# Optimization experiments

Measured on AMD Instinct MI355X. Metric: run time of the kernel, lower is better.

The kernel has to match this reference:

```python
import jax, jax.numpy as jnp
import numpy as np

HIDDEN = 1024


def setup_inputs() -> dict:
    key = jax.random.key(0)
    ks = jax.random.split(key, 9)
    B, S, Kq, H = 16, 4096, 64, HIDDEN
    scale = 1.0 / np.sqrt(H)
    return {
        "queries": jax.random.normal(ks[0], (B, Kq, H), jnp.float32),
        "keys": jax.random.normal(ks[1], (B, S, H), jnp.float32),
        "values": jax.random.normal(ks[2], (B, S, H), jnp.float32),
        "Wq": jax.random.normal(ks[3], (H, H), jnp.float32) * scale,
        "bq": jax.random.normal(ks[4], (H,), jnp.float32) * 0.02,
        "Wk": jax.random.normal(ks[5], (H, H), jnp.float32) * scale,
        "bk": jax.random.normal(ks[6], (H,), jnp.float32) * 0.02,
        "Wv": jax.random.normal(ks[7], (H, H), jnp.float32) * scale,
        "bv": jax.random.normal(ks[8], (H,), jnp.float32) * 0.02,
    }


def reference(queries, keys, values, Wq, bq, Wk, bk, Wv, bv):
    H = Wq.shape[0]
    scaling = jax.lax.rsqrt(jnp.asarray(H, queries.dtype))
    # torch Linear: x @ W^T + b
    q = queries @ Wq.T + bq            # (B, Kq, H)
    k = keys @ Wk.T + bk               # (B, S, H)
    v = values @ Wv.T + bv             # (B, S, H)
    # scores: k @ q^T -> (B, S, Kq), softmax over seq_len axis (dim=1)
    scores = jnp.einsum('bsh,bqh->bsq', k, q) * scaling
    attention_weights = jax.nn.softmax(scores, axis=1)
    # context: attn^T @ v -> (B, Kq, H)
    context = jnp.einsum('bsq,bsh->bqh', attention_weights, v)
    return context, attention_weights
```

## Files before the change

kernel.cpp:

```cpp
#include <hip/hip_runtime.h>
#include <hip/hip_bf16.h>

#define H 1024
#define SEQ 4096
#define BQ 64
#define NB 16

typedef float f32x4 __attribute__((ext_vector_type(4)));
typedef __bf16 bf16x8 __attribute__((ext_vector_type(8)));

__device__ __forceinline__ void split_bf16(const float* x, bf16x8& hi, bf16x8& lo)
{
    #pragma unroll
    for (int i = 0; i < 8; ++i) {
        float v = x[i];
        __bf16 h = (__bf16)v;
        hi[i] = h;
        lo[i] = (__bf16)(v - (float)h);
    }
}

__device__ __forceinline__ void gload_lds16(const float* g, void* lds)
{
    __builtin_amdgcn_global_load_lds(
        (const __attribute__((address_space(1))) void*)g,
        (__attribute__((address_space(3))) void*)lds, 16, 0, 0);
}

template<int MODE>
__global__ __launch_bounds__(512)
void gemm_bt_512(const float* __restrict__ A, const float* __restrict__ Bm,
                 const float* __restrict__ bias, float* __restrict__ C,
                 __bf16* __restrict__ Nhi, __bf16* __restrict__ Nlo, float scale)
{
    const int m0 = blockIdx.x * 64;
    const int n0 = blockIdx.y * 64;
    const int t   = threadIdx.x;
    const int w   = t >> 6;
    const int wm  = w & 3;
    const int kh  = w >> 2;
    const int l   = t & 63;
    const int row = l & 15;
    const int kg  = l >> 4;

    const float* ap = A + (size_t)(m0 + wm * 16 + row) * H + kh * 512 + kg * 8;
    const float* bp = Bm + (size_t)(n0 + row) * H + kh * 512 + kg * 8;

    f32x4 acc[4] = {};
    for (int k0 = 0; k0 < 512; k0 += 32) {
        float a8[8];
        *reinterpret_cast<float4*>(&a8[0]) = *reinterpret_cast<const float4*>(ap + k0);
        *reinterpret_cast<float4*>(&a8[4]) = *reinterpret_cast<const float4*>(ap + k0 + 4);
        bf16x8 ahi, alo;
        split_bf16(a8, ahi, alo);
        #pragma unroll
        for (int j = 0; j < 4; ++j) {
            float b8[8];
            const float* bjp = bp + (size_t)j * 16 * H + k0;
            *reinterpret_cast<float4*>(&b8[0]) = *reinterpret_cast<const float4*>(bjp);
            *reinterpret_cast<float4*>(&b8[4]) = *reinterpret_cast<const float4*>(bjp + 4);
            bf16x8 bhi, blo;
            split_bf16(b8, bhi, blo);
            acc[j] = __builtin_amdgcn_mfma_f32_16x16x32_bf16(ahi, bhi, acc[j], 0, 0, 0);
            acc[j] = __builtin_amdgcn_mfma_f32_16x16x32_bf16(ahi, blo, acc[j], 0, 0, 0);
            acc[j] = __builtin_amdgcn_mfma_f32_16x16x32_bf16(alo, bhi, acc[j], 0, 0, 0);
        }
    }

    __shared__ f32x4 red[4][4][64];
    if (kh == 1) {
        #pragma unroll
        for (int j = 0; j < 4; ++j) red[wm][j][l] = acc[j];
    }
    __syncthreads();
    if (kh == 0) {
        #pragma unroll
        for (int j = 0; j < 4; ++j) {
            f32x4 s = acc[j] + red[wm][j][l];
            int n = n0 + j * 16 + row;
            if (MODE == 0) {
                float bb = bias ? bias[n] : 0.f;
                #pragma unroll
                for (int r = 0; r < 4; ++r) {
                    int m = m0 + wm * 16 + kg * 4 + r;
                    C[(size_t)m * H + n] = s[r] * scale + bb;
                }
            } else {
                #pragma unroll
                for (int r = 0; r < 4; ++r) {
                    int m = m0 + wm * 16 + kg * 4 + r;
                    float v = s[r] * scale;
                    __bf16 hi = (__bf16)v;
                    Nhi[(size_t)m * H + n] = hi;
                    Nlo[(size_t)m * H + n] = (__bf16)(v - (float)hi);
                }
            }
        }
    }
}

__global__ __launch_bounds__(256)
void transpose_k(const float* __restrict__ Wk, float* __restrict__ WkT)
{
    __shared__ float tile[64][65];
    const int k0 = blockIdx.x * 64;
    const int n0 = blockIdx.y * 64;
    const int t  = threadIdx.x;
    const int c4 = (t & 15) * 4;
    const int r  = t >> 4;
    #pragma unroll
    for (int p = 0; p < 4; ++p) {
        float4 v = *reinterpret_cast<const float4*>(&Wk[(size_t)(k0 + r + 16 * p) * H + n0 + c4]);
        tile[r + 16 * p][c4 + 0] = v.x;
        tile[r + 16 * p][c4 + 1] = v.y;
        tile[r + 16 * p][c4 + 2] = v.z;
        tile[r + 16 * p][c4 + 3] = v.w;
    }
    __syncthreads();
    #pragma unroll
    for (int p = 0; p < 4; ++p) {
        int rr = r + 16 * p;
        float4 o;
        o.x = tile[c4 + 0][rr];
        o.y = tile[c4 + 1][rr];
        o.z = tile[c4 + 2][rr];
        o.w = tile[c4 + 3][rr];
        *reinterpret_cast<float4*>(&WkT[(size_t)(n0 + rr) * H + k0 + c4]) = o;
    }
}

__global__ __launch_bounds__(256)
void cvec_kernel(const float* __restrict__ q, const float* __restrict__ bk,
                 float* __restrict__ cvec, float scale)
{
    int r = blockIdx.x * 4 + (threadIdx.x >> 6);
    int l = threadIdx.x & 63;
    float s = 0.f;
    #pragma unroll
    for (int i = 0; i < 16; ++i)
        s += q[(size_t)r * H + l + 64 * i] * bk[l + 64 * i];
    #pragma unroll
    for (int off = 32; off; off >>= 1)
        s += __shfl_down(s, off);
    if (l == 0) cvec[r] = s * scale;
}

__global__ __launch_bounds__(512)
void scores_mfma(const float* __restrict__ keys,
                 const __bf16* __restrict__ Nhi, const __bf16* __restrict__ Nlo,
                 const float* __restrict__ cvec, float* __restrict__ scores,
                 float* __restrict__ pmax, float* __restrict__ psum)
{
    const int id = blockIdx.x;
    const int x  = id & 7;
    const int m  = id >> 3;
    const int b  = 2 * x + (m >> 5);
    const int ch = m & 31;
    const int s0 = ch * 128;

    const int t   = threadIdx.x;
    const int w   = t >> 6;
    const int l   = t & 63;
    const int row = l & 15;
    const int kg  = l >> 4;

    __shared__ __bf16 nshH[64][16][8];
    __shared__ __bf16 nshL[64][16][8];
    __shared__ float redm[8][64];

    const float* ka = keys + ((size_t)b * SEQ + s0 + w * 16 + row) * H + kg * 8;
    const __bf16* nhb = Nhi + (size_t)b * BQ * H;
    const __bf16* nlb = Nlo + (size_t)b * BQ * H;

    const int sqi = (t >> 4) & 31;
    const int skb = t & 15;
    const int ssl = skb ^ (sqi & 7);

    f32x4 acc[4] = {};
    for (int c = 0; c < 8; ++c) {
        const int kc = c * 128;
        float4 kr[8];
        #pragma unroll
        for (int ii = 0; ii < 4; ++ii) {
            kr[2 * ii + 0] = *reinterpret_cast<const float4*>(ka + kc + ii * 32);
            kr[2 * ii + 1] = *reinterpret_cast<const float4*>(ka + kc + ii * 32 + 4);
        }
        bf16x8 nh[2], nl[2];
        #pragma unroll
        for (int rep = 0; rep < 2; ++rep) {
            size_t go = (size_t)(rep * 32 + sqi) * H + kc + skb * 8;
            nh[rep] = *reinterpret_cast<const bf16x8*>(nhb + go);
            nl[rep] = *reinterpret_cast<const bf16x8*>(nlb + go);
        }
        __syncthreads();
        #pragma unroll
        for (int rep = 0; rep < 2; ++rep) {
            *reinterpret_cast<bf16x8*>(&nshH[rep * 32 + sqi][ssl][0]) = nh[rep];
            *reinterpret_cast<bf16x8*>(&nshL[rep * 32 + sqi][ssl][0]) = nl[rep];
        }
        __syncthreads();
        #pragma unroll
        for (int ii = 0; ii < 4; ++ii) {
            float a8[8];
            *reinterpret_cast<float4*>(&a8[0]) = kr[2 * ii + 0];
            *reinterpret_cast<float4*>(&a8[4]) = kr[2 * ii + 1];
            bf16x8 ahi, alo;
            split_bf16(a8, ahi, alo);
            const int kb = ii * 4 + kg;
            const int slot = kb ^ (row & 7);
            #pragma unroll
            for (int j = 0; j < 4; ++j) {
                const int qi = j * 16 + row;
                bf16x8 bhi = *reinterpret_cast<const bf16x8*>(&nshH[qi][slot][0]);
                bf16x8 blo = *reinterpret_cast<const bf16x8*>(&nshL[qi][slot][0]);
                acc[j] = __builtin_amdgcn_mfma_f32_16x16x32_bf16(ahi, bhi, acc[j], 0, 0, 0);
                acc[j] = __builtin_amdgcn_mfma_f32_16x16x32_bf16(ahi, blo, acc[j], 0, 0, 0);
                acc[j] = __builtin_amdgcn_mfma_f32_16x16x32_bf16(alo, bhi, acc[j], 0, 0, 0);
            }
        }
    }

    #pragma unroll
    for (int j = 0; j < 4; ++j) {
        int qi = j * 16 + row;
        float cv = cvec[b * BQ + qi];
        #pragma unroll
        for (int r = 0; r < 4; ++r) {
            acc[j][r] += cv;
            int s = s0 + w * 16 + kg * 4 + r;
            scores[((size_t)b * SEQ + s) * BQ + qi] = acc[j][r];
        }
    }
    float mj[4];
    #pragma unroll
    for (int j = 0; j < 4; ++j) {
        float mm = fmaxf(fmaxf(acc[j][0], acc[j][1]), fmaxf(acc[j][2], acc[j][3]));
        mm = fmaxf(mm, __shfl_xor(mm, 16));
        mm = fmaxf(mm, __shfl_xor(mm, 32));
        mj[j] = mm;
    }
    __syncthreads();
    if (kg == 0) {
        #pragma unroll
        for (int j = 0; j < 4; ++j) redm[w][j * 16 + row] = mj[j];
    }
    __syncthreads();
    float Mj[4];
    #pragma unroll
    for (int j = 0; j < 4; ++j) {
        const int qi = j * 16 + row;
        float M = redm[0][qi];
        #pragma unroll
        for (int ww = 1; ww < 8; ++ww) M = fmaxf(M, redm[ww][qi]);
        Mj[j] = M;
    }
    float sj[4];
    #pragma unroll
    for (int j = 0; j < 4; ++j) {
        float s = 0.f;
        #pragma unroll
        for (int r = 0; r < 4; ++r) s += __expf(acc[j][r] - Mj[j]);
        s += __shfl_xor(s, 16);
        s += __shfl_xor(s, 32);
        sj[j] = s;
    }
    __syncthreads();
    if (kg == 0) {
        #pragma unroll
        for (int j = 0; j < 4; ++j) redm[w][j * 16 + row] = sj[j];
    }
    __syncthreads();
    if (w == 0 && kg == 0) {
        #pragma unroll
        for (int j = 0; j < 4; ++j) {
            const int qi = j * 16 + row;
            float ss = 0.f;
            #pragma unroll
            for (int ww = 0; ww < 8; ++ww) ss += redm[ww][qi];
            pmax[((size_t)b * 32 + ch) * 64 + qi] = Mj[j];
            psum[((size_t)b * 32 + ch) * 64 + qi] = ss;
        }
    }
}

__global__ void sm_combine(const float* __restrict__ pmax,
                           const float* __restrict__ psum,
                           float* __restrict__ gstat)
{
    int b  = blockIdx.x;
    int qi = threadIdx.x;
    float m = -1e30f;
    for (int c = 0; c < 32; ++c)
        m = fmaxf(m, pmax[((size_t)b * 32 + c) * 64 + qi]);
    float s = 0.f;
    for (int c = 0; c < 32; ++c)
        s += psum[((size_t)b * 32 + c) * 64 + qi] *
             __expf(pmax[((size_t)b * 32 + c) * 64 + qi] - m);
    gstat[(size_t)b * 64 + qi] = m;
    gstat[(size_t)(NB + b) * 64 + qi] = 1.f / s;
}

__global__ __launch_bounds__(256)
void sm_norm(float* __restrict__ attn, const float* __restrict__ gstat,
             __hip_bfloat16* __restrict__ abfT)
{
    __shared__ float tile[64][133];
    const int b  = blockIdx.y;
    const int ch = blockIdx.x;
    const int t  = threadIdx.x;
    const int qi = t & 63;
    const int g  = t >> 6;
    const float M   = gstat[(size_t)b * 64 + qi];
    const float inv = gstat[(size_t)(NB + b) * 64 + qi];
    float* sb = attn + ((size_t)b * SEQ + ch * 128) * BQ;
    #pragma unroll 8
    for (int i = 0; i < 32; ++i) {
        int sl = g + i * 4;
        size_t idx = (size_t)sl * BQ + qi;
        float w = __expf(sb[idx] - M) * inv;
        sb[idx] = w;
        tile[qi][sl] = w;
    }
    __syncthreads();
    const int qo = t >> 2;
    const int c  = (t & 3) * 32;
    __hip_bfloat16* dst = abfT + ((size_t)(b * BQ + qo)) * SEQ + ch * 128 + c;
    #pragma unroll
    for (int v = 0; v < 4; ++v) {
        bf16x8 w8;
        #pragma unroll
        for (int e = 0; e < 8; ++e)
            w8[e] = (__bf16)tile[qo][c + v * 8 + e];
        *reinterpret_cast<bf16x8*>(dst + v * 8) = w8;
    }
}

template<int SC>
__global__ __launch_bounds__(256)
void tmat_mfma(const __hip_bfloat16* __restrict__ abfT,
               const float* __restrict__ values,
               float* __restrict__ Tpart)
{
    const int i  = blockIdx.x;
    const int h0 = ((i >> 3) & 7) * 128;
    const int g  = (i & 7) + 8 * (i >> 6);
    const int b  = g / SC;
    const int sc = g % SC;
    const int schunk = SEQ / SC;

    const int w   = threadIdx.x >> 6;
    const int l   = threadIdx.x & 63;
    const int row = l & 15;
    const int kg  = l >> 4;
    const int sbase = sc * schunk;

    __shared__ float vlds[2][32][128];

    const __hip_bfloat16* ap = abfT + ((size_t)b * BQ + row) * SEQ + sbase + kg * 8;
    const float* vb = values + ((size_t)b * SEQ + sbase) * H + h0;

    const int nk = schunk / 32;

    #define STAGE(buf, k0)                                                     \
        {                                                                      \
            _Pragma("unroll")                                                  \
            for (int ii = 0; ii < 4; ++ii) {                                   \
                int elem = w * 1024 + ii * 256 + l * 4;                        \
                int k    = elem >> 7;                                          \
                int cc   = elem & 127;                                         \
                int csw  = cc ^ ((k >> 3) << 4);                               \
                const float* src = vb + (size_t)((k0) + k) * H + csw;          \
                gload_lds16(src, (void*)(&vlds[buf][0][0] + w * 1024 + ii * 256)); \
            }                                                                  \
        }

    f32x4 acc[4][2] = {};
    STAGE(0, 0);
    __syncthreads();

    for (int ks = 0; ks < nk; ++ks) {
        const int buf = ks & 1;
        if (ks + 1 < nk) STAGE(buf ^ 1, (ks + 1) * 32);
        const int k0 = ks * 32;
        bf16x8 a[4];
        #pragma unroll
        for (int q = 0; q < 4; ++q)
            a[q] = *reinterpret_cast<const bf16x8*>(ap + (size_t)q * 16 * SEQ + k0);
        #pragma unroll
        for (int j = 0; j < 2; ++j) {
            const int col = (w * 32 + j * 16 + row) ^ (kg << 4);
            float b8[8];
            #pragma unroll
            for (int e = 0; e < 8; ++e)
                b8[e] = vlds[buf][kg * 8 + e][col];
            bf16x8 bhi, blo;
            split_bf16(b8, bhi, blo);
            #pragma unroll
            for (int q = 0; q < 4; ++q) {
                acc[q][j] = __builtin_amdgcn_mfma_f32_16x16x32_bf16(a[q], bhi, acc[q][j], 0, 0, 0);
                acc[q][j] = __builtin_amdgcn_mfma_f32_16x16x32_bf16(a[q], blo, acc[q][j], 0, 0, 0);
            }
        }
        __syncthreads();
    }
    #undef STAGE

    float* tp = Tpart + ((size_t)sc * NB + b) * BQ * H;
    #pragma unroll
    for (int q = 0; q < 4; ++q) {
        #pragma unroll
        for (int j = 0; j < 2; ++j) {
            int h = h0 + w * 32 + j * 16 + row;
            #pragma unroll
            for (int r = 0; r < 4; ++r) {
                int qi = q * 16 + kg * 4 + r;
                tp[(size_t)qi * H + h] = acc[q][j][r];
            }
        }
    }
}

template<int SC>
__global__ __launch_bounds__(256)
void tsum_kernel(float* __restrict__ Tpart)
{
    const size_t stride = (size_t)NB * BQ * H;
    size_t i = ((size_t)blockIdx.x * 256 + threadIdx.x) * 4;
    f32x4 s = *reinterpret_cast<const f32x4*>(Tpart + i);
    #pragma unroll
    for (int p = 1; p < SC; ++p)
        s += *reinterpret_cast<const f32x4*>(Tpart + p * stride + i);
    *reinterpret_cast<f32x4*>(Tpart + i) = s;
}

extern "C" void kernel_launch(void* const* d_in, const int* in_sizes, int n_in,
                              void* d_out, int out_size, void* d_ws, size_t ws_size,
                              hipStream_t stream)
{
    const float* queries = (const float*)d_in[0];
    const float* keys    = (const float*)d_in[1];
    const float* values  = (const float*)d_in[2];
    const float* Wq = (const float*)d_in[3];
    const float* bq = (const float*)d_in[4];
    const float* Wk = (const float*)d_in[5];
    const float* bk = (const float*)d_in[6];
    const float* Wv = (const float*)d_in[7];
    const float* bv = (const float*)d_in[8];

    float* out     = (float*)d_out;
    float* context = out;
    float* attn    = out + (size_t)NB * BQ * H;

    const int SC = (ws_size >= (41ull << 20)) ? 8 : 2;

    char* ws = (char*)d_ws;
    float* q     = (float*)ws;
    float* WkT   = (float*)(ws + (4ull << 20));
    __bf16* Nhi  = (__bf16*)(ws + (8ull << 20));
    __bf16* Nlo  = (__bf16*)(ws + (10ull << 20));
    float* Tpart = (float*)ws;
    __hip_bfloat16* abfT = (__hip_bfloat16*)(ws + (size_t)SC * (4ull << 20));
    char* smalls = ws + (size_t)SC * (4ull << 20) + (8ull << 20);
    float* cvec  = (float*)smalls;
    float* gstat = (float*)(smalls + (64u << 10));
    float* pmax  = (float*)(smalls + (128u << 10));
    float* psum  = (float*)(smalls + (512u << 10));

    const float scale = 0.03125f;

    transpose_k<<<dim3(16, 16), 256, 0, stream>>>(Wk, WkT);
    gemm_bt_512<0><<<dim3(16, 16), 512, 0, stream>>>(
        queries, Wq, bq, q, nullptr, nullptr, 1.0f);
    gemm_bt_512<1><<<dim3(16, 16), 512, 0, stream>>>(
        q, WkT, nullptr, nullptr, Nhi, Nlo, scale);
    cvec_kernel<<<256, 256, 0, stream>>>(q, bk, cvec, scale);
    scores_mfma<<<512, 512, 0, stream>>>(keys, Nhi, Nlo, cvec, attn, pmax, psum);
    sm_combine<<<NB, 64, 0, stream>>>(pmax, psum, gstat);
    sm_norm<<<dim3(32, NB), 256, 0, stream>>>(attn, gstat, abfT);
    if (SC == 8) tmat_mfma<8><<<8 * NB * 8, 256, 0, stream>>>(abfT, values, Tpart);
    else         tmat_mfma<2><<<8 * NB * 2, 256, 0, stream>>>(abfT, values, Tpart);
    if (SC == 8) tsum_kernel<8><<<1024, 256, 0, stream>>>(Tpart);
    else         tsum_kernel<2><<<1024, 256, 0, stream>>>(Tpart);
    gemm_bt_512<0><<<dim3(16, 16), 512, 0, stream>>>(
        Tpart, Wv, bv, context, nullptr, nullptr, 1.0f);
}
```

Baseline: 284.8 us.

## Fuse small kernels, drop Wk transpose, double-buffer scores k-loop

```diff
diff --git a/kernel.cpp b/kernel.cpp
--- a/kernel.cpp
+++ b/kernel.cpp
@@ -27,11 +27,12 @@
         (__attribute__((address_space(3))) void*)lds, 16, 0, 0);
 }
 
-template<int MODE>
+template<bool CVEC>
 __global__ __launch_bounds__(512)
 void gemm_bt_512(const float* __restrict__ A, const float* __restrict__ Bm,
                  const float* __restrict__ bias, float* __restrict__ C,
-                 __bf16* __restrict__ Nhi, __bf16* __restrict__ Nlo, float scale)
+                 float scale, const float* __restrict__ bk,
+                 float* __restrict__ cvec, float cscale)
 {
     const int m0 = blockIdx.x * 64;
     const int n0 = blockIdx.y * 64;
@@ -74,78 +75,99 @@
     }
     __syncthreads();
     if (kh == 0) {
+        float p[4] = {0.f, 0.f, 0.f, 0.f};
         #pragma unroll
         for (int j = 0; j < 4; ++j) {
             f32x4 s = acc[j] + red[wm][j][l];
             int n = n0 + j * 16 + row;
-            if (MODE == 0) {
-                float bb = bias ? bias[n] : 0.f;
+            float bb = bias ? bias[n] : 0.f;
+            float bkv = CVEC ? bk[n] : 0.f;
+            #pragma unroll
+            for (int r = 0; r < 4; ++r) {
+                int m = m0 + wm * 16 + kg * 4 + r;
+                float o = s[r] * scale + bb;
+                C[(size_t)m * H + n] = o;
+                if (CVEC) p[r] += o * bkv;
+            }
+        }
+        if (CVEC) {
+            #pragma unroll
+            for (int r = 0; r < 4; ++r) {
                 #pragma unroll
-                for (int r = 0; r < 4; ++r) {
-                    int m = m0 + wm * 16 + kg * 4 + r;
-                    C[(size_t)m * H + n] = s[r] * scale + bb;
-                }
-            } else {
+                for (int off = 1; off < 16; off <<= 1)
+                    p[r] += __shfl_xor(p[r], off);
+            }
+            if (row == 0) {
                 #pragma unroll
-                for (int r = 0; r < 4; ++r) {
-                    int m = m0 + wm * 16 + kg * 4 + r;
-                    float v = s[r] * scale;
-                    __bf16 hi = (__bf16)v;
-                    Nhi[(size_t)m * H + n] = hi;
-                    Nlo[(size_t)m * H + n] = (__bf16)(v - (float)hi);
-                }
-            }
-        }
-    }
-}
-
-__global__ __launch_bounds__(256)
-void transpose_k(const float* __restrict__ Wk, float* __restrict__ WkT)
-{
-    __shared__ float tile[64][65];
-    const int k0 = blockIdx.x * 64;
+                for (int r = 0; r < 4; ++r)
+                    atomicAdd(&cvec[m0 + wm * 16 + kg * 4 + r], p[r] * cscale);
+            }
+        }
+    }
+}
+
+__global__ __launch_bounds__(512)
+void ngemm_direct(const float* __restrict__ A, const float* __restrict__ Wk,
+                  __bf16* __restrict__ Nhi, __bf16* __restrict__ Nlo, float scale)
+{
+    const int m0 = blockIdx.x * 64;
     const int n0 = blockIdx.y * 64;
-    const int t  = threadIdx.x;
-    const int c4 = (t & 15) * 4;
-    const int r  = t >> 4;
-    #pragma unroll
-    for (int p = 0; p < 4; ++p) {
-        float4 v = *reinterpret_cast<const float4*>(&Wk[(size_t)(k0 + r + 16 * p) * H + n0 + c4]);
-        tile[r + 16 * p][c4 + 0] = v.x;
-        tile[r + 16 * p][c4 + 1] = v.y;
-        tile[r + 16 * p][c4 + 2] = v.z;
-        tile[r + 16 * p][c4 + 3] = v.w;
-    }
-    __syncthreads();
-    #pragma unroll
-    for (int p = 0; p < 4; ++p) {
-        int rr = r + 16 * p;
-        float4 o;
-        o.x = tile[c4 + 0][rr];
-        o.y = tile[c4 + 1][rr];
-        o.z = tile[c4 + 2][rr];
-        o.w = tile[c4 + 3][rr];
-        *reinterpret_cast<float4*>(&WkT[(size_t)(n0 + rr) * H + k0 + c4]) = o;
-    }
-}
-
-__global__ __launch_bounds__(256)
-void cvec_kernel(const float* __restrict__ q, const float* __restrict__ bk,
-                 float* __restrict__ cvec, float scale)
-{
-    int r = blockIdx.x * 4 + (threadIdx.x >> 6);
-    int l = threadIdx.x & 63;
-    float s = 0.f;
-    #pragma unroll
-    for (int i = 0; i < 16; ++i)
-        s += q[(size_t)r * H + l + 64 * i] * bk[l + 64 * i];
-    #pragma unroll
-    for (int off = 32; off; off >>= 1)
-        s += __shfl_down(s, off);
-    if (l == 0) cvec[r] = s * scale;
-}
-
-__global__ __launch_bounds__(512)
+    const int t   = threadIdx.x;
+    const int w   = t >> 6;
+    const int wm  = w & 3;
+    const int kh  = w >> 2;
+    const int l   = t & 63;
+    const int row = l & 15;
+    const int kg  = l >> 4;
+
+    const float* ap = A + (size_t)(m0 + wm * 16 + row) * H + kh * 512 + kg * 8;
+    const float* bp = Wk + (size_t)(kh * 512 + kg * 8) * H + n0 + row;
+
+    f32x4 acc[4] = {};
+    for (int k0 = 0; k0 < 512; k0 += 32) {
+        float a8[8];
+        *reinterpret_cast<float4*>(&a8[0]) = *reinterpret_cast<const float4*>(ap + k0);
+        *reinterpret_cast<float4*>(&a8[4]) = *reinterpret_cast<const float4*>(ap + k0 + 4);
+        bf16x8 ahi, alo;
+        split_bf16(a8, ahi, alo);
+        #pragma unroll
+        for (int j = 0; j < 4; ++j) {
+            float b8[8];
+            #pragma unroll
+            for (int e = 0; e < 8; ++e)
+                b8[e] = bp[(size_t)(k0 + e) * H + j * 16];
+            bf16x8 bhi, blo;
+            split_bf16(b8, bhi, blo);
+            acc[j] = __builtin_amdgcn_mfma_f32_16x16x32_bf16(ahi, bhi, acc[j], 0, 0, 0);
+            acc[j] = __builtin_amdgcn_mfma_f32_16x16x32_bf16(ahi, blo, acc[j], 0, 0, 0);
+            acc[j] = __builtin_amdgcn_mfma_f32_16x16x32_bf16(alo, bhi, acc[j], 0, 0, 0);
+        }
+    }
+
+    __shared__ f32x4 red[4][4][64];
+    if (kh == 1) {
+        #pragma unroll
+        for (int j = 0; j < 4; ++j) red[wm][j][l] = acc[j];
+    }
+    __syncthreads();
+    if (kh == 0) {
+        #pragma unroll
+        for (int j = 0; j < 4; ++j) {
+            f32x4 s = acc[j] + red[wm][j][l];
+            int n = n0 + j * 16 + row;
+            #pragma unroll
+            for (int r = 0; r < 4; ++r) {
+                int m = m0 + wm * 16 + kg * 4 + r;
+                float v = s[r] * scale;
+                __bf16 hi = (__bf16)v;
+                Nhi[(size_t)m * H + n] = hi;
+                Nlo[(size_t)m * H + n] = (__bf16)(v - (float)hi);
+            }
+        }
+    }
+}
+
+__global__ __launch_bounds__(512, 4)
 void scores_mfma(const float* __restrict__ keys,
                  const __bf16* __restrict__ Nhi, const __bf16* __restrict__ Nlo,
                  const float* __restrict__ cvec, float* __restrict__ scores,
@@ -164,46 +186,54 @@
     const int row = l & 15;
     const int kg  = l >> 4;
 
-    __shared__ __bf16 nshH[64][16][8];
-    __shared__ __bf16 nshL[64][16][8];
+    __shared__ __bf16 nshH[2][64][8][8];
+    __shared__ __bf16 nshL[2][64][8][8];
     __shared__ float redm[8][64];
 
     const float* ka = keys + ((size_t)b * SEQ + s0 + w * 16 + row) * H + kg * 8;
     const __bf16* nhb = Nhi + (size_t)b * BQ * H;
     const __bf16* nlb = Nlo + (size_t)b * BQ * H;
 
-    const int sqi = (t >> 4) & 31;
-    const int skb = t & 15;
+    const int sqi = t >> 3;
+    const int skb = t & 7;
     const int ssl = skb ^ (sqi & 7);
 
+    float4 kr[2][4];
+    bf16x8 nh[2], nl[2];
+    #pragma unroll
+    for (int ii = 0; ii < 2; ++ii) {
+        kr[0][2 * ii + 0] = *reinterpret_cast<const float4*>(ka + ii * 32);
+        kr[0][2 * ii + 1] = *reinterpret_cast<const float4*>(ka + ii * 32 + 4);
+    }
+    {
+        size_t go = (size_t)sqi * H + skb * 8;
+        nh[0] = *reinterpret_cast<const bf16x8*>(nhb + go);
+        nl[0] = *reinterpret_cast<const bf16x8*>(nlb + go);
+    }
+
     f32x4 acc[4] = {};
-    for (int c = 0; c < 8; ++c) {
-        const int kc = c * 128;
-        float4 kr[8];
-        #pragma unroll
-        for (int ii = 0; ii < 4; ++ii) {
-            kr[2 * ii + 0] = *reinterpret_cast<const float4*>(ka + kc + ii * 32);
-            kr[2 * ii + 1] = *reinterpret_cast<const float4*>(ka + kc + ii * 32 + 4);
-        }
-        bf16x8 nh[2], nl[2];
-        #pragma unroll
-        for (int rep = 0; rep < 2; ++rep) {
-            size_t go = (size_t)(rep * 32 + sqi) * H + kc + skb * 8;
-            nh[rep] = *reinterpret_cast<const bf16x8*>(nhb + go);
-            nl[rep] = *reinterpret_cast<const bf16x8*>(nlb + go);
-        }
+    #pragma unroll
+    for (int c = 0; c < 16; ++c) {
+        const int buf = c & 1;
+        *reinterpret_cast<bf16x8*>(&nshH[buf][sqi][ssl][0]) = nh[buf];
+        *reinterpret_cast<bf16x8*>(&nshL[buf][sqi][ssl][0]) = nl[buf];
         __syncthreads();
-        #pragma unroll
-        for (int rep = 0; rep < 2; ++rep) {
-            *reinterpret_cast<bf16x8*>(&nshH[rep * 32 + sqi][ssl][0]) = nh[rep];
-            *reinterpret_cast<bf16x8*>(&nshL[rep * 32 + sqi][ssl][0]) = nl[rep];
-        }
-        __syncthreads();
-        #pragma unroll
-        for (int ii = 0; ii < 4; ++ii) {
+        if (c < 15) {
+            const int kc = (c + 1) * 64;
+            #pragma unroll
+            for (int ii = 0; ii < 2; ++ii) {
+                kr[buf ^ 1][2 * ii + 0] = *reinterpret_cast<const float4*>(ka + kc + ii * 32);
+                kr[buf ^ 1][2 * ii + 1] = *reinterpret_cast<const float4*>(ka + kc + ii * 32 + 4);
+            }
+            size_t go = (size_t)sqi * H + kc + skb * 8;
+            nh[buf ^ 1] = *reinterpret_cast<const bf16x8*>(nhb + go);
+            nl[buf ^ 1] = *reinterpret_cast<const bf16x8*>(nlb + go);
+        }
+        #pragma unroll
+        for (int ii = 0; ii < 2; ++ii) {
             float a8[8];
-            *reinterpret_cast<float4*>(&a8[0]) = kr[2 * ii + 0];
-            *reinterpret_cast<float4*>(&a8[4]) = kr[2 * ii + 1];
+            *reinterpret_cast<float4*>(&a8[0]) = kr[buf][2 * ii + 0];
+            *reinterpret_cast<float4*>(&a8[4]) = kr[buf][2 * ii + 1];
             bf16x8 ahi, alo;
             split_bf16(a8, ahi, alo);
             const int kb = ii * 4 + kg;
@@ -211,8 +241,8 @@
             #pragma unroll
             for (int j = 0; j < 4; ++j) {
                 const int qi = j * 16 + row;
-                bf16x8 bhi = *reinterpret_cast<const bf16x8*>(&nshH[qi][slot][0]);
-                bf16x8 blo = *reinterpret_cast<const bf16x8*>(&nshL[qi][slot][0]);
+                bf16x8 bhi = *reinterpret_cast<const bf16x8*>(&nshH[buf][qi][slot][0]);
+                bf16x8 blo = *reinterpret_cast<const bf16x8*>(&nshL[buf][qi][slot][0]);
                 acc[j] = __builtin_amdgcn_mfma_f32_16x16x32_bf16(ahi, bhi, acc[j], 0, 0, 0);
                 acc[j] = __builtin_amdgcn_mfma_f32_16x16x32_bf16(ahi, blo, acc[j], 0, 0, 0);
                 acc[j] = __builtin_amdgcn_mfma_f32_16x16x32_bf16(alo, bhi, acc[j], 0, 0, 0);
@@ -283,26 +313,9 @@
     }
 }
 
-__global__ void sm_combine(const float* __restrict__ pmax,
-                           const float* __restrict__ psum,
-                           float* __restrict__ gstat)
-{
-    int b  = blockIdx.x;
-    int qi = threadIdx.x;
-    float m = -1e30f;
-    for (int c = 0; c < 32; ++c)
-        m = fmaxf(m, pmax[((size_t)b * 32 + c) * 64 + qi]);
-    float s = 0.f;
-    for (int c = 0; c < 32; ++c)
-        s += psum[((size_t)b * 32 + c) * 64 + qi] *
-             __expf(pmax[((size_t)b * 32 + c) * 64 + qi] - m);
-    gstat[(size_t)b * 64 + qi] = m;
-    gstat[(size_t)(NB + b) * 64 + qi] = 1.f / s;
-}
-
 __global__ __launch_bounds__(256)
-void sm_norm(float* __restrict__ attn, const float* __restrict__ gstat,
-             __hip_bfloat16* __restrict__ abfT)
+void sm_norm(float* __restrict__ attn, const float* __restrict__ pmax,
+             const float* __restrict__ psum, __hip_bfloat16* __restrict__ abfT)
 {
     __shared__ float tile[64][133];
     const int b  = blockIdx.y;
@@ -310,8 +323,18 @@
     const int t  = threadIdx.x;
     const int qi = t & 63;
     const int g  = t >> 6;
-    const float M   = gstat[(size_t)b * 64 + qi];
-    const float inv = gstat[(size_t)(NB + b) * 64 + qi];
+
+    float M = -1e30f;
+    #pragma unroll 4
+    for (int c = 0; c < 32; ++c)
+        M = fmaxf(M, pmax[((size_t)b * 32 + c) * 64 + qi]);
+    float ssum = 0.f;
+    #pragma unroll 4
+    for (int c = 0; c < 32; ++c)
+        ssum += psum[((size_t)b * 32 + c) * 64 + qi] *
+                __expf(pmax[((size_t)b * 32 + c) * 64 + qi] - M);
+    const float inv = 1.f / ssum;
+
     float* sb = attn + ((size_t)b * SEQ + ch * 128) * BQ;
     #pragma unroll 8
     for (int i = 0; i < 32; ++i) {
@@ -455,32 +478,27 @@
 
     char* ws = (char*)d_ws;
     float* q     = (float*)ws;
-    float* WkT   = (float*)(ws + (4ull << 20));
     __bf16* Nhi  = (__bf16*)(ws + (8ull << 20));
     __bf16* Nlo  = (__bf16*)(ws + (10ull << 20));
     float* Tpart = (float*)ws;
     __hip_bfloat16* abfT = (__hip_bfloat16*)(ws + (size_t)SC * (4ull << 20));
     char* smalls = ws + (size_t)SC * (4ull << 20) + (8ull << 20);
     float* cvec  = (float*)smalls;
-    float* gstat = (float*)(smalls + (64u << 10));
     float* pmax  = (float*)(smalls + (128u << 10));
     float* psum  = (float*)(smalls + (512u << 10));
 
     const float scale = 0.03125f;
 
-    transpose_k<<<dim3(16, 16), 256, 0, stream>>>(Wk, WkT);
-    gemm_bt_512<0><<<dim3(16, 16), 512, 0, stream>>>(
-        queries, Wq, bq, q, nullptr, nullptr, 1.0f);
-    gemm_bt_512<1><<<dim3(16, 16), 512, 0, stream>>>(
-        q, WkT, nullptr, nullptr, Nhi, Nlo, scale);
-    cvec_kernel<<<256, 256, 0, stream>>>(q, bk, cvec, scale);
+    hipMemsetAsync(cvec, 0, (size_t)NB * BQ * sizeof(float), stream);
+    gemm_bt_512<true><<<dim3(16, 16), 512, 0, stream>>>(
+        queries, Wq, bq, q, 1.0f, bk, cvec, scale);
+    ngemm_direct<<<dim3(16, 16), 512, 0, stream>>>(q, Wk, Nhi, Nlo, scale);
     scores_mfma<<<512, 512, 0, stream>>>(keys, Nhi, Nlo, cvec, attn, pmax, psum);
-    sm_combine<<<NB, 64, 0, stream>>>(pmax, psum, gstat);
-    sm_norm<<<dim3(32, NB), 256, 0, stream>>>(attn, gstat, abfT);
+    sm_norm<<<dim3(32, NB), 256, 0, stream>>>(attn, pmax, psum, abfT);
     if (SC == 8) tmat_mfma<8><<<8 * NB * 8, 256, 0, stream>>>(abfT, values, Tpart);
     else         tmat_mfma<2><<<8 * NB * 2, 256, 0, stream>>>(abfT, values, Tpart);
     if (SC == 8) tsum_kernel<8><<<1024, 256, 0, stream>>>(Tpart);
     else         tsum_kernel<2><<<1024, 256, 0, stream>>>(Tpart);
-    gemm_bt_512<0><<<dim3(16, 16), 512, 0, stream>>>(
-        Tpart, Wv, bv, context, nullptr, nullptr, 1.0f);
-}
+    gemm_bt_512<false><<<dim3(16, 16), 512, 0, stream>>>(
+        Tpart, Wv, bv, context, 1.0f, nullptr, nullptr, 0.f);
+}
```

Measured after the change: 281.8 us (median of 2 runs). Within noise of the previous version (-1.0%).
